# Kernel tuning notes

Measured on AMD Instinct MI355X. Metric: run time of the kernel, lower is better.

## Reference

```python
import jax, jax.numpy as jnp
import numpy as np

EPS = 1e-5
NUM_HEADS = 8
GN_GROUPS = 32


def _hardswish(x):
    return x * jnp.clip(x + 3.0, 0.0, 6.0) / 6.0


def setup_inputs() -> dict:
    key = jax.random.key(0)
    ks = jax.random.split(key, 12)
    B, C, H, W = 2, 256, 56, 56
    mid, inner = 32, 64  # mid_ca=max(C//8,32); inner=max(C//8, 8*8)//8*8
    s = 0.02
    return {
        "x": jax.random.normal(ks[0], (B, C, H, W), jnp.float32),
        "gate_conv_w": jax.random.normal(ks[1], (mid, C), jnp.float32) * s,
        "bn_gamma": jnp.ones((mid,), jnp.float32),
        "bn_beta": jnp.zeros((mid,), jnp.float32),
        "bn_mean": jax.random.normal(ks[2], (mid,), jnp.float32) * 0.1,
        "bn_var": jax.random.uniform(ks[3], (mid,), jnp.float32) + 0.5,
        "gate_h_w": jax.random.normal(ks[4], (C, mid), jnp.float32) * s,
        "gate_w_w": jax.random.normal(ks[5], (C, mid), jnp.float32) * s,
        "proj_in_w": jax.random.normal(ks[6], (inner, C), jnp.float32) * s,
        "ln_gamma": jnp.ones((inner,), jnp.float32),
        "ln_beta": jnp.zeros((inner,), jnp.float32),
        "wq": jax.random.normal(ks[7], (inner, inner), jnp.float32) * s,
        "wk": jax.random.normal(ks[8], (inner, inner), jnp.float32) * s,
        "wv": jax.random.normal(ks[9], (inner, inner), jnp.float32) * s,
        "proj_out_w": jax.random.normal(ks[10], (C, inner), jnp.float32) * s,
        "gn_gamma": jnp.ones((C,), jnp.float32),
        "gn_beta": jnp.zeros((C,), jnp.float32),
    }


def reference(x, gate_conv_w, bn_gamma, bn_beta, bn_mean, bn_var,
              gate_h_w, gate_w_w, proj_in_w, ln_gamma, ln_beta,
              wq, wk, wv, proj_out_w, gn_gamma, gn_beta):
    B, C, H, W = x.shape
    N = H * W
    inner = proj_in_w.shape[0]
    dh = inner // NUM_HEADS
    scale = dh ** (-0.5)

    # ---- CA gate: pool along W and H, shared 1x1 conv + BN(eval) + hardswish ----
    h_pool = x.mean(axis=3)                      # (B,C,H)
    w_pool = x.mean(axis=2)                      # (B,C,W)
    cat = jnp.concatenate([h_pool, w_pool], axis=2)          # (B,C,H+W)
    cat = jnp.einsum('mc,bcl->bml', gate_conv_w, cat)        # 1x1 conv
    cat = (cat - bn_mean[:, None]) * jax.lax.rsqrt(bn_var[:, None] + EPS)
    cat = cat * bn_gamma[:, None] + bn_beta[:, None]
    cat = _hardswish(cat)
    g_h, g_w = cat[:, :, :H], cat[:, :, H:]                  # (B,mid,H), (B,mid,W)
    gate_h = jax.nn.sigmoid(jnp.einsum('cm,bmh->bch', gate_h_w, g_h))  # (B,C,H)
    gate_w = jax.nn.sigmoid(jnp.einsum('cm,bmw->bcw', gate_w_w, g_w))  # (B,C,W)
    gate = gate_h[:, :, :, None] * gate_w[:, :, None, :]     # (B,C,H,W)

    # ---- projection + layernorm over channel dim ----
    seq = jnp.einsum('ic,bchw->bhwi', proj_in_w, x).reshape(B, N, inner)
    mu = seq.mean(-1, keepdims=True)
    var = seq.var(-1, keepdims=True)  # biased, as torch LayerNorm
    seq = (seq - mu) * jax.lax.rsqrt(var + EPS) * ln_gamma + ln_beta

    gate_spatial = gate.mean(axis=1).reshape(B, N)           # (B,N)

    def heads(w):
        return (seq @ w.T).reshape(B, N, NUM_HEADS, dh).transpose(0, 2, 1, 3)
    q, k, v = heads(wq), heads(wk), heads(wv)                # (B,h,N,dh)

    scores = jnp.einsum('bhnd,bhmd->bhnm', q, k) * scale     # (B,h,N,N)
    gate_bias = jnp.maximum(jnp.log(gate_spatial), -5.0)[:, None, None, :]
    attn = jax.nn.softmax(scores + gate_bias, axis=-1)
    out = jnp.einsum('bhnm,bhmd->bhnd', attn, v)             # (B,h,N,dh)
    out = out.transpose(0, 2, 1, 3).reshape(B, N, inner)
    out = out.transpose(0, 2, 1).reshape(B, inner, H, W)
    out = jnp.einsum('ci,bihw->bchw', proj_out_w, out)       # proj_out 1x1 conv

    # ---- GroupNorm(32, C) ----
    og = out.reshape(B, GN_GROUPS, C // GN_GROUPS, H, W)
    gmu = og.mean((2, 3, 4), keepdims=True)
    gvar = og.var((2, 3, 4), keepdims=True)
    og = (og - gmu) * jax.lax.rsqrt(gvar + EPS)
    out = og.reshape(B, C, H, W) * gn_gamma[None, :, None, None] + gn_beta[None, :, None, None]

    return x + out
```

## Files before the change

### kernel.cpp

```cpp
#include <hip/hip_runtime.h>
#include <math.h>

#define EPSF 1e-5f

constexpr int B_ = 2, C_ = 256, H_ = 56, W_ = 56, N_ = 3136;
constexpr int MID_ = 32, L_ = 112, IN_ = 64, NH_ = 8;

typedef __attribute__((ext_vector_type(8))) __bf16 bf16x8;
typedef __attribute__((ext_vector_type(16))) float f32x16;

constexpr size_t O_POOL = 0;
constexpr size_t O_CAT  = O_POOL + (size_t)B_*C_*L_;
constexpr size_t O_GH   = O_CAT  + (size_t)B_*MID_*L_;
constexpr size_t O_GW   = O_GH   + (size_t)B_*C_*H_;
constexpr size_t O_BIAS = O_GW   + (size_t)B_*C_*W_;
constexpr size_t O_QT   = O_BIAS + (size_t)B_*N_;
constexpr size_t O_KT   = O_QT   + (size_t)B_*NH_*N_*16/2;
constexpr size_t O_VT   = O_KT   + (size_t)B_*NH_*N_*16/2;
constexpr size_t O_VZ   = O_VT   + (size_t)B_*NH_*16*N_/2;
constexpr size_t O_AOT  = O_VZ   + N_/2;
constexpr size_t O_OUTC = O_AOT  + (size_t)B_*N_*IN_;
constexpr size_t O_GST  = O_OUTC + (size_t)B_*C_*N_;
constexpr size_t O_PART = O_GST  + (size_t)B_*32*2;

__device__ inline unsigned pkbf(float lo, float hi) {
  __bf16 a = (__bf16)lo, c = (__bf16)hi;
  return (unsigned)__builtin_bit_cast(unsigned short, a)
       | ((unsigned)__builtin_bit_cast(unsigned short, c) << 16);
}

__device__ inline float fast_exp2(float x) {
#if __has_builtin(__builtin_amdgcn_exp2f)
  return __builtin_amdgcn_exp2f(x);
#else
  float r; asm("v_exp_f32 %0, %1" : "=v"(r) : "v"(x)); return r;
#endif
}

__device__ inline void plane32_swap(unsigned &a, unsigned &b) {
#if __has_builtin(__builtin_amdgcn_permlane32_swap)
  typedef unsigned uv2 __attribute__((ext_vector_type(2)));
  uv2 r = __builtin_amdgcn_permlane32_swap(a, b, false, false);
  a = r.x; b = r.y;
#else
  asm volatile("v_permlane32_swap_b32 %0, %1" : "+v"(a), "+v"(b));
#endif
}

__global__ __launch_bounds__(256) void k_pool(const float* __restrict__ x, float* __restrict__ pool) {
  int bc = blockIdx.x;
  const float4* xp4 = reinterpret_cast<const float4*>(x + (size_t)bc * N_);
  __shared__ float tile[N_];
  float4* t4 = reinterpret_cast<float4*>(tile);
  for (int i = threadIdx.x; i < N_/4; i += 256) t4[i] = xp4[i];
  __syncthreads();
  int t = threadIdx.x;
  if (t < 224) {
    int o = t >> 1, half = t & 1;
    float r = 0.f;
    if (o < 56) {
      const float* row = tile + o*W_ + half*28;
      #pragma unroll 7
      for (int j = 0; j < 28; ++j) r += row[j];
    } else {
      const float* col = tile + (half*28)*W_ + (o - 56);
      #pragma unroll 7
      for (int j = 0; j < 28; ++j) r += col[j*W_];
    }
    r += __shfl_xor(r, 1);
    if (half == 0) pool[(size_t)bc*L_ + o] = r * (1.f/56.f);
  }
}

__global__ __launch_bounds__(256) void k_gates2(const float* __restrict__ gcw, const float* __restrict__ pool,
    const float* __restrict__ bng, const float* __restrict__ bnb,
    const float* __restrict__ bnm, const float* __restrict__ bnv,
    const float* __restrict__ ghw, const float* __restrict__ gww,
    float* __restrict__ ghT, float* __restrict__ gwT) {
  int b = blockIdx.x / H_;
  int p = blockIdx.x % H_;
  __shared__ float cat_s[2][MID_];
  int t = threadIdx.x;
  {
    int out = t >> 2, sub = t & 3;
    int m = out & 31, which = out >> 5;
    int l = p + which*H_;
    const float* pp = pool + (size_t)b*C_*L_ + l;
    const float* wp = gcw + (size_t)m*C_ + sub*64;
    float s = 0.f;
    #pragma unroll 16
    for (int c = 0; c < 64; ++c) s += wp[c] * pp[(size_t)(sub*64 + c)*L_];
    s += __shfl_xor(s, 1); s += __shfl_xor(s, 2);
    if (sub == 0) {
      float xn = (s - bnm[m]) * rsqrtf(bnv[m] + EPSF) * bng[m] + bnb[m];
      cat_s[which][m] = xn * fminf(fmaxf(xn + 3.f, 0.f), 6.f) * (1.f/6.f);
    }
  }
  __syncthreads();
  int c = t;
  float sh = 0.f, sw = 0.f;
  #pragma unroll 8
  for (int m = 0; m < MID_; ++m) {
    sh += ghw[c*MID_ + m] * cat_s[0][m];
    sw += gww[c*MID_ + m] * cat_s[1][m];
  }
  ghT[((size_t)b*H_ + p)*C_ + c] = 1.f/(1.f + expf(-sh));
  gwT[((size_t)b*W_ + p)*C_ + c] = 1.f/(1.f + expf(-sw));
}

__global__ __launch_bounds__(256) void k_bias(const float* __restrict__ ghT, const float* __restrict__ gwT,
                                              float* __restrict__ bias) {
  int wid = blockIdx.x*4 + (threadIdx.x >> 6);
  int lane = threadIdx.x & 63;
  int n = wid % N_, b = wid / N_;
  int h = n / W_, w = n % W_;
  float4 a  = *reinterpret_cast<const float4*>(ghT + ((size_t)b*H_ + h)*C_ + lane*4);
  float4 c2 = *reinterpret_cast<const float4*>(gwT + ((size_t)b*W_ + w)*C_ + lane*4);
  float s = a.x*c2.x + a.y*c2.y + a.z*c2.z + a.w*c2.w;
  s += __shfl_xor(s, 1);  s += __shfl_xor(s, 2);  s += __shfl_xor(s, 4);
  s += __shfl_xor(s, 8);  s += __shfl_xor(s, 16); s += __shfl_xor(s, 32);
  if (lane == 0)
    bias[(size_t)b*N_ + n] = fmaxf(logf(s * (1.f/C_)), -5.f) * 1.4426950408889634f;
}

__global__ __launch_bounds__(256) void k_fused(const float* __restrict__ x,
    const float* __restrict__ piw, const float* __restrict__ lng, const float* __restrict__ lnb,
    const float* __restrict__ wq, const float* __restrict__ wk, const float* __restrict__ wv,
    const float* __restrict__ bias,
    unsigned short* __restrict__ qt, unsigned short* __restrict__ kt,
    unsigned short* __restrict__ vt, unsigned short* __restrict__ vz) {
  __shared__ __align__(16) unsigned short sT[64][72];
  __shared__ float ps[2][2][64][2];
  __shared__ float lg[64], lb[64];
  int b = blockIdx.x / 49, n0 = (blockIdx.x % 49) * 64;
  int tid = threadIdx.x;
  int wv_ = tid >> 6, lane = tid & 63;
  int m = wv_ & 1, nh = wv_ >> 1, l31 = lane & 31, g = lane >> 5;
  int nloc = nh*32 + l31;
  int nglob = n0 + nloc;
  const float QS = 0.35355339059327373f * 1.4426950408889634f;

  if (tid < 64) { lg[tid] = lng[tid]; lb[tid] = lnb[tid]; }

  for (int u = tid; u < 512; u += 256) {
    int h = u >> 6, n = u & 63;
    size_t base = ((size_t)(b*NH_ + h)*N_ + n0 + n)*16;
    *reinterpret_cast<uint4*>(qt + base + 8) = make_uint4(0x3F803F80u, 0u, 0u, 0u);
    float bv = bias[(size_t)b*N_ + n0 + n];
    __bf16 bhi = (__bf16)bv; float blo = bv - (float)bhi;
    *reinterpret_cast<uint4*>(kt + base + 8) = make_uint4(pkbf((float)bhi, blo), 0u, 0u, 0u);
  }
  for (int u = tid; u < 512; u += 256) {
    int rr = u >> 3, chunk = u & 7;
    int h = rr >> 3, r = 8 + (rr & 7);
    unsigned val = (r == 8 || r == 12) ? 0x3F803F80u : 0u;
    *reinterpret_cast<uint4*>(vt + ((size_t)(b*NH_+h)*16 + r)*N_ + n0 + chunk*8)
        = make_uint4(val, val, val, val);
  }
  if (b == 0 && tid < 8)
    *reinterpret_cast<uint4*>(vz + n0 + tid*8) = make_uint4(0u, 0u, 0u, 0u);

  const float* arow = piw + (size_t)(32*m + l31)*C_;
  const float* xcol = x + (size_t)b*C_*N_ + nglob;
  f32x16 acc;
  #pragma unroll
  for (int i = 0; i < 16; ++i) acc[i] = 0.f;
  #pragma unroll 4
  for (int kk = 0; kk < 16; ++kk) {
    const float4* ap = reinterpret_cast<const float4*>(arow + kk*16 + g*8);
    float4 a0 = ap[0], a1 = ap[1];
    uint4 au;
    au.x = pkbf(a0.x, a0.y); au.y = pkbf(a0.z, a0.w);
    au.z = pkbf(a1.x, a1.y); au.w = pkbf(a1.z, a1.w);
    float bvl[8];
    #pragma unroll
    for (int e = 0; e < 8; ++e) bvl[e] = xcol[(size_t)(kk*16 + g*8 + e)*N_];
    uint4 bu;
    bu.x = pkbf(bvl[0], bvl[1]); bu.y = pkbf(bvl[2], bvl[3]);
    bu.z = pkbf(bvl[4], bvl[5]); bu.w = pkbf(bvl[6], bvl[7]);
    acc = __builtin_amdgcn_mfma_f32_32x32x16_bf16(
        __builtin_bit_cast(bf16x8, au), __builtin_bit_cast(bf16x8, bu), acc, 0, 0, 0);
  }

  float s = 0.f, ss = 0.f;
  #pragma unroll
  for (int i = 0; i < 16; ++i) { s += acc[i]; ss += acc[i]*acc[i]; }
  ps[m][g][nloc][0] = s; ps[m][g][nloc][1] = ss;
  __syncthreads();
  float S  = ps[0][0][nloc][0] + ps[0][1][nloc][0] + ps[1][0][nloc][0] + ps[1][1][nloc][0];
  float SS = ps[0][0][nloc][1] + ps[0][1][nloc][1] + ps[1][0][nloc][1] + ps[1][1][nloc][1];
  float mu = S * (1.f/IN_);
  float var = SS * (1.f/IN_) - mu*mu;
  float rsd = rsqrtf(var + EPSF);

  #pragma unroll
  for (int cg = 0; cg < 4; ++cg) {
    int jb = 8*cg + 4*g + 32*m;
    float v0 = (acc[cg*4+0]-mu)*rsd*lg[jb+0] + lb[jb+0];
    float v1 = (acc[cg*4+1]-mu)*rsd*lg[jb+1] + lb[jb+1];
    float v2 = (acc[cg*4+2]-mu)*rsd*lg[jb+2] + lb[jb+2];
    float v3 = (acc[cg*4+3]-mu)*rsd*lg[jb+3] + lb[jb+3];
    uint2 w; w.x = pkbf(v0, v1); w.y = pkbf(v2, v3);
    *reinterpret_cast<uint2*>(&sT[nloc][jb]) = w;
  }
  __syncthreads();

  f32x16 aq, ak, av;
  #pragma unroll
  for (int i = 0; i < 16; ++i) { aq[i] = 0.f; ak[i] = 0.f; av[i] = 0.f; }
  const float* qrw = wq + (size_t)(32*m + l31)*IN_;
  const float* krw = wk + (size_t)(32*m + l31)*IN_;
  const float* vrw = wv + (size_t)(32*m + l31)*IN_;
  #pragma unroll
  for (int kk = 0; kk < 4; ++kk) {
    bf16x8 bfr = __builtin_bit_cast(bf16x8,
        *reinterpret_cast<const uint4*>(&sT[nloc][kk*16 + g*8]));
    auto ldA = [&](const float* wrow) {
      const float4* fp = reinterpret_cast<const float4*>(wrow + kk*16 + g*8);
      float4 f0 = fp[0], f1 = fp[1];
      uint4 u;
      u.x = pkbf(f0.x, f0.y); u.y = pkbf(f0.z, f0.w);
      u.z = pkbf(f1.x, f1.y); u.w = pkbf(f1.z, f1.w);
      return __builtin_bit_cast(bf16x8, u);
    };
    aq = __builtin_amdgcn_mfma_f32_32x32x16_bf16(ldA(qrw), bfr, aq, 0, 0, 0);
    ak = __builtin_amdgcn_mfma_f32_32x32x16_bf16(ldA(krw), bfr, ak, 0, 0, 0);
    av = __builtin_amdgcn_mfma_f32_32x32x16_bf16(ldA(vrw), bfr, av, 0, 0, 0);
  }

  #pragma unroll
  for (int cg = 0; cg < 4; ++cg) {
    int h = 4*m + cg, d0 = 4*g;
    size_t rb = ((size_t)(b*NH_ + h)*N_ + nglob)*16 + d0;
    uint2 wqv;
    wqv.x = pkbf(aq[cg*4+0]*QS, aq[cg*4+1]*QS);
    wqv.y = pkbf(aq[cg*4+2]*QS, aq[cg*4+3]*QS);
    *reinterpret_cast<uint2*>(qt + rb) = wqv;
    uint2 wkv;
    wkv.x = pkbf(ak[cg*4+0], ak[cg*4+1]);
    wkv.y = pkbf(ak[cg*4+2], ak[cg*4+3]);
    *reinterpret_cast<uint2*>(kt + rb) = wkv;
    unsigned r0 = pkbf(av[cg*4+0], av[cg*4+1]);
    unsigned r1 = pkbf(av[cg*4+2], av[cg*4+3]);
    size_t vb0 = ((size_t)(b*NH_+h)*16 + d0)*N_ + nglob;
    vt[vb0]                = (unsigned short)r0;
    vt[vb0 + N_]           = (unsigned short)(r0 >> 16);
    vt[vb0 + 2*(size_t)N_] = (unsigned short)r1;
    vt[vb0 + 3*(size_t)N_] = (unsigned short)(r1 >> 16);
  }
}

__global__ __launch_bounds__(256, 4) void k_attn7(const unsigned short* __restrict__ qt,
    const unsigned short* __restrict__ kt, const unsigned short* __restrict__ vt,
    const unsigned short* __restrict__ vz, float* __restrict__ part_g) {
  int tid = threadIdx.x;
  int lane = tid & 63, kh = tid >> 6;
  int l31 = lane & 31, g = lane >> 5;
  int bh = blockIdx.x & 15;
  int rest = blockIdx.x >> 4;
  int qti = rest >> 1, half = rest & 1;
  int qbase = qti * 64;

  bf16x8 qfA = __builtin_bit_cast(bf16x8,
      *reinterpret_cast<const uint4*>(qt + ((size_t)bh*N_ + qbase + l31)*16 + g*8));
  bf16x8 qfB = __builtin_bit_cast(bf16x8,
      *reinterpret_cast<const uint4*>(qt + ((size_t)bh*N_ + qbase + 32 + l31)*16 + g*8));
  f32x16 zf, accA, accB;
  #pragma unroll
  for (int i = 0; i < 16; ++i) { zf[i] = 0.f; accA[i] = 0.f; accB[i] = 0.f; }
  const unsigned short* krow = kt + (size_t)bh*N_*16 + g*8;
  const unsigned short* vbase = (l31 < 16) ? (vt + ((size_t)bh*16 + l31)*(size_t)N_) : vz;

  auto ld = [&](const unsigned short* p) {
    return __builtin_bit_cast(bf16x8, *reinterpret_cast<const uint4*>(p));
  };
  auto halfstep = [&](const f32x16& sa, f32x16& acc, bf16x8 v1, bf16x8 v2) {
    float p[16];
    #pragma unroll
    for (int r = 0; r < 16; ++r) p[r] = fast_exp2(sa[r]);
    unsigned u01 = pkbf(p[0],p[1]),  u23 = pkbf(p[2],p[3]);
    unsigned u45 = pkbf(p[4],p[5]),  u67 = pkbf(p[6],p[7]);
    unsigned u89 = pkbf(p[8],p[9]),  uab = pkbf(p[10],p[11]);
    unsigned ucd = pkbf(p[12],p[13]), uef = pkbf(p[14],p[15]);
    plane32_swap(u01, u45);
    plane32_swap(u23, u67);
    plane32_swap(u89, ucd);
    plane32_swap(uab, uef);
    bf16x8 pf1 = __builtin_bit_cast(bf16x8, make_uint4(u01, u23, u45, u67));
    bf16x8 pf2 = __builtin_bit_cast(bf16x8, make_uint4(u89, uab, ucd, uef));
    acc = __builtin_amdgcn_mfma_f32_32x32x16_bf16(v1, pf1, acc, 0, 0, 0);
    acc = __builtin_amdgcn_mfma_f32_32x32x16_bf16(v2, pf2, acc, 0, 0, 0);
  };

  int tb0 = (half*49 + kh*12) * 32;
  const unsigned short* kp  = krow  + (size_t)(tb0 + l31)*16;
  const unsigned short* vp1 = vbase + tb0 + g*8;
  const unsigned short* vp2 = vp1 + 16;

  bf16x8 kfN = ld(kp), v1N = ld(vp1), v2N = ld(vp2);
  #pragma unroll 4
  for (int j = 0; j < 12; ++j) {
    bf16x8 kf = kfN, v1 = v1N, v2 = v2N;
    if (j < 11) {
      kfN = ld(kp  + (size_t)(j+1)*512);
      v1N = ld(vp1 + (j+1)*32);
      v2N = ld(vp2 + (j+1)*32);
    }
    f32x16 sA = __builtin_amdgcn_mfma_f32_32x32x16_bf16(kf, qfA, zf, 0, 0, 0);
    f32x16 sB = __builtin_amdgcn_mfma_f32_32x32x16_bf16(kf, qfB, zf, 0, 0, 0);
    halfstep(sA, accA, v1, v2);
    halfstep(sB, accB, v1, v2);
  }
  if (kh == 0) {
    int tb = (half*49 + 48) * 32;
    bf16x8 kf = ld(krow + (size_t)(tb + l31)*16);
    bf16x8 v1 = ld(vbase + tb + g*8);
    bf16x8 v2 = ld(vbase + tb + 16 + g*8);
    f32x16 sA = __builtin_amdgcn_mfma_f32_32x32x16_bf16(kf, qfA, zf, 0, 0, 0);
    f32x16 sB = __builtin_amdgcn_mfma_f32_32x32x16_bf16(kf, qfB, zf, 0, 0, 0);
    halfstep(sA, accA, v1, v2);
    halfstep(sB, accB, v1, v2);
  }

  __shared__ float part[3][2][64][5];
  if (kh > 0) {
    #pragma unroll
    for (int j = 0; j < 5; ++j) {
      part[kh-1][0][lane][j] = accA[j];
      part[kh-1][1][lane][j] = accB[j];
    }
  }
  __syncthreads();
  if (kh == 0) {
    float rA[5], rB[5];
    #pragma unroll
    for (int j = 0; j < 5; ++j) { rA[j] = accA[j]; rB[j] = accB[j]; }
    #pragma unroll
    for (int c = 0; c < 3; ++c) {
      #pragma unroll
      for (int j = 0; j < 5; ++j) {
        rA[j] += part[c][0][lane][j];
        rB[j] += part[c][1][lane][j];
      }
    }
    float* pg = part_g + ((((size_t)half*16 + bh)*2 + g)*5)*N_ + qbase + l31;
    #pragma unroll
    for (int j = 0; j < 5; ++j) {
      pg[(size_t)j*N_]      = rA[j];
      pg[(size_t)j*N_ + 32] = rB[j];
    }
  }
}

__global__ __launch_bounds__(128) void k_proj3(const float* __restrict__ part_g,
    const float* __restrict__ pw, float* __restrict__ outc, float* __restrict__ gst) {
  int bid = blockIdx.x;
  int nb = bid % 49, ct = (bid / 49) % 8, b = bid / (49*8);
  int wave = threadIdx.x >> 6, lane = threadIdx.x & 63;
  int l31 = lane & 31, g = lane >> 5;
  int n0 = nb*64, c0 = ct*32;
  int nw = n0 + wave*32;

  __shared__ float invs[8][64];
  for (int u = threadIdx.x; u < 512; u += 128) {
    int h = u >> 6, n = u & 63;
    size_t r0 = ((((size_t)0*16 + b*8 + h)*2 + 0)*5 + 4)*N_ + n0 + n;
    size_t r1 = ((((size_t)1*16 + b*8 + h)*2 + 0)*5 + 4)*N_ + n0 + n;
    invs[h][n] = 1.f / (part_g[r0] + part_g[r1]);
  }
  __syncthreads();

  const float* wrow = pw + (size_t)(c0 + l31)*IN_;
  bf16x8 afr[4];
  #pragma unroll
  for (int kk = 0; kk < 4; ++kk) {
    const float4* fp = reinterpret_cast<const float4*>(wrow + kk*16 + g*8);
    float4 f0 = fp[0], f1 = fp[1];
    uint4 u;
    u.x = pkbf(f0.x, f0.y); u.y = pkbf(f0.z, f0.w);
    u.z = pkbf(f1.x, f1.y); u.w = pkbf(f1.z, f1.w);
    afr[kk] = __builtin_bit_cast(bf16x8, u);
  }

  f32x16 acc;
  #pragma unroll
  for (int i = 0; i < 16; ++i) acc[i] = 0.f;
  #pragma unroll
  for (int kk = 0; kk < 4; ++kk) {
    int h = kk*2 + g;
    float iv = invs[h][wave*32 + l31];
    const float* p0 = part_g + (((size_t)0*16 + b*8 + h)*2)*5*N_ + nw + l31;
    const float* p1 = part_g + (((size_t)1*16 + b*8 + h)*2)*5*N_ + nw + l31;
    unsigned words[4];
    #pragma unroll
    for (int ep = 0; ep < 4; ++ep) {
      float vv[2];
      #pragma unroll
      for (int e2 = 0; e2 < 2; ++e2) {
        int d = ep*2 + e2;
        int gr = d >> 2, j = d & 3;
        size_t off = ((size_t)gr*5 + j)*N_;
        vv[e2] = (p0[off] + p1[off]) * iv;
      }
      words[ep] = pkbf(vv[0], vv[1]);
    }
    uint4 bu = make_uint4(words[0], words[1], words[2], words[3]);
    acc = __builtin_amdgcn_mfma_f32_32x32x16_bf16(afr[kk], __builtin_bit_cast(bf16x8, bu), acc, 0, 0, 0);
  }

  float* op = outc + ((size_t)b*C_ + c0)*N_ + nw + l31;
  #pragma unroll
  for (int reg = 0; reg < 16; ++reg) {
    int row = (reg & 3) + 8*(reg >> 2) + 4*g;
    op[(size_t)row*N_] = acc[reg];
  }

  float s4[4], q4[4];
  #pragma unroll
  for (int gl = 0; gl < 4; ++gl) {
    s4[gl] = acc[gl*4+0] + acc[gl*4+1] + acc[gl*4+2] + acc[gl*4+3];
    q4[gl] = acc[gl*4+0]*acc[gl*4+0] + acc[gl*4+1]*acc[gl*4+1]
           + acc[gl*4+2]*acc[gl*4+2] + acc[gl*4+3]*acc[gl*4+3];
  }
  #pragma unroll
  for (int gl = 0; gl < 4; ++gl) {
    #pragma unroll
    for (int off = 32; off > 0; off >>= 1) {
      s4[gl] += __shfl_xor(s4[gl], off);
      q4[gl] += __shfl_xor(q4[gl], off);
    }
  }
  __shared__ float red[2][4][2];
  if (lane == 0) {
    #pragma unroll
    for (int gl = 0; gl < 4; ++gl) { red[wave][gl][0] = s4[gl]; red[wave][gl][1] = q4[gl]; }
  }
  __syncthreads();
  if (threadIdx.x < 8) {
    int gl = threadIdx.x >> 1, which = threadIdx.x & 1;
    float v = red[0][gl][which] + red[1][gl][which];
    atomicAdd(&gst[((size_t)b*32 + ct*4 + gl)*2 + which], v);
  }
}

__global__ __launch_bounds__(256) void k_final(const float* __restrict__ x, const float* __restrict__ outc,
    const float* __restrict__ gst, const float* __restrict__ gng, const float* __restrict__ gnb,
    float* __restrict__ out) {
  int tid = blockIdx.x*256 + threadIdx.x;
  size_t idx = (size_t)tid * 4;
  int c = (int)((idx / N_) % C_);
  int b = (int)(idx / ((size_t)C_*N_));
  int g = c >> 3;
  float S  = gst[(b*32+g)*2];
  float SS = gst[(b*32+g)*2+1];
  const float invn = 1.f/(8.f*N_);
  float mu = S * invn;
  float var = SS * invn - mu*mu;
  float rs = rsqrtf(var + EPSF);
  float ga = gng[c], be = gnb[c];
  float4 xv = *reinterpret_cast<const float4*>(x + idx);
  float4 ov = *reinterpret_cast<const float4*>(outc + idx);
  float4 r;
  r.x = xv.x + (ov.x - mu)*rs*ga + be;
  r.y = xv.y + (ov.y - mu)*rs*ga + be;
  r.z = xv.z + (ov.z - mu)*rs*ga + be;
  r.w = xv.w + (ov.w - mu)*rs*ga + be;
  *reinterpret_cast<float4*>(out + idx) = r;
}

extern "C" void kernel_launch(void* const* d_in, const int* in_sizes, int n_in,
                              void* d_out, int out_size, void* d_ws, size_t ws_size,
                              hipStream_t stream) {
  const float* x   = (const float*)d_in[0];
  const float* gcw = (const float*)d_in[1];
  const float* bng = (const float*)d_in[2];
  const float* bnb = (const float*)d_in[3];
  const float* bnm = (const float*)d_in[4];
  const float* bnv = (const float*)d_in[5];
  const float* ghw = (const float*)d_in[6];
  const float* gww = (const float*)d_in[7];
  const float* piw = (const float*)d_in[8];
  const float* lng = (const float*)d_in[9];
  const float* lnb = (const float*)d_in[10];
  const float* wq  = (const float*)d_in[11];
  const float* wk  = (const float*)d_in[12];
  const float* wv  = (const float*)d_in[13];
  const float* pw  = (const float*)d_in[14];
  const float* gng = (const float*)d_in[15];
  const float* gnb = (const float*)d_in[16];
  float* ws  = (float*)d_ws;
  float* out = (float*)d_out;
  unsigned short* qt  = (unsigned short*)(ws + O_QT);
  unsigned short* kt  = (unsigned short*)(ws + O_KT);
  unsigned short* vt  = (unsigned short*)(ws + O_VT);
  unsigned short* vz  = (unsigned short*)(ws + O_VZ);

  hipMemsetAsync(ws + O_GST, 0, (size_t)B_*32*2*sizeof(float), stream);
  k_pool<<<B_*C_, 256, 0, stream>>>(x, ws + O_POOL);
  k_gates2<<<B_*H_, 256, 0, stream>>>(gcw, ws+O_POOL, bng, bnb, bnm, bnv, ghw, gww, ws+O_GH, ws+O_GW);
  k_bias<<<(B_*N_)/4, 256, 0, stream>>>(ws+O_GH, ws+O_GW, ws+O_BIAS);
  k_fused<<<B_*49, 256, 0, stream>>>(x, piw, lng, lnb, wq, wk, wv, ws+O_BIAS, qt, kt, vt, vz);
  k_attn7<<<16*98, 256, 0, stream>>>(qt, kt, vt, vz, ws+O_PART);
  k_proj3<<<B_*8*49, 128, 0, stream>>>(ws+O_PART, pw, ws+O_OUTC, ws+O_GST);
  k_final<<<(B_*C_*N_)/(4*256), 256, 0, stream>>>(x, ws+O_OUTC, ws+O_GST, gng, gnb, out);
}
```

Baseline: 84.14 us.

## Fuse gate bias into k_fused, drop memset, store proj_out in bf16

Folds the spatial gate-bias computation into k_fused: each block computes its 64 pixels' bias from ghT/gwT into shared memory. This removes the k_bias launch and its global round trip. The GroupNorm stats buffer is now zeroed inside k_fused instead of by a separate memset. The proj_out intermediate is stored as bf16 instead of fp32, halving its write and read traffic in k_proj3 and k_final. The risk is some precision loss in the residual output, while the GroupNorm stats stay computed from fp32 accumulators.

```diff
diff --git a/kernel.cpp b/kernel.cpp
--- a/kernel.cpp
+++ b/kernel.cpp
@@ -10,23 +10,25 @@
 typedef __attribute__((ext_vector_type(16))) float f32x16;
 
 constexpr size_t O_POOL = 0;
-constexpr size_t O_CAT  = O_POOL + (size_t)B_*C_*L_;
-constexpr size_t O_GH   = O_CAT  + (size_t)B_*MID_*L_;
+constexpr size_t O_GH   = O_POOL + (size_t)B_*C_*L_;
 constexpr size_t O_GW   = O_GH   + (size_t)B_*C_*H_;
-constexpr size_t O_BIAS = O_GW   + (size_t)B_*C_*W_;
-constexpr size_t O_QT   = O_BIAS + (size_t)B_*N_;
+constexpr size_t O_QT   = O_GW   + (size_t)B_*C_*W_;
 constexpr size_t O_KT   = O_QT   + (size_t)B_*NH_*N_*16/2;
 constexpr size_t O_VT   = O_KT   + (size_t)B_*NH_*N_*16/2;
 constexpr size_t O_VZ   = O_VT   + (size_t)B_*NH_*16*N_/2;
-constexpr size_t O_AOT  = O_VZ   + N_/2;
-constexpr size_t O_OUTC = O_AOT  + (size_t)B_*N_*IN_;
-constexpr size_t O_GST  = O_OUTC + (size_t)B_*C_*N_;
+constexpr size_t O_OUTC = O_VZ   + N_/2;
+constexpr size_t O_GST  = O_OUTC + (size_t)B_*C_*N_/2;
 constexpr size_t O_PART = O_GST  + (size_t)B_*32*2;
 
 __device__ inline unsigned pkbf(float lo, float hi) {
   __bf16 a = (__bf16)lo, c = (__bf16)hi;
   return (unsigned)__builtin_bit_cast(unsigned short, a)
        | ((unsigned)__builtin_bit_cast(unsigned short, c) << 16);
+}
+
+__device__ inline float bf2f(unsigned short u) {
+  unsigned v = (unsigned)u << 16;
+  return __builtin_bit_cast(float, v);
 }
 
 __device__ inline float fast_exp2(float x) {
@@ -108,30 +110,17 @@
   gwT[((size_t)b*W_ + p)*C_ + c] = 1.f/(1.f + expf(-sw));
 }
 
-__global__ __launch_bounds__(256) void k_bias(const float* __restrict__ ghT, const float* __restrict__ gwT,
-                                              float* __restrict__ bias) {
-  int wid = blockIdx.x*4 + (threadIdx.x >> 6);
-  int lane = threadIdx.x & 63;
-  int n = wid % N_, b = wid / N_;
-  int h = n / W_, w = n % W_;
-  float4 a  = *reinterpret_cast<const float4*>(ghT + ((size_t)b*H_ + h)*C_ + lane*4);
-  float4 c2 = *reinterpret_cast<const float4*>(gwT + ((size_t)b*W_ + w)*C_ + lane*4);
-  float s = a.x*c2.x + a.y*c2.y + a.z*c2.z + a.w*c2.w;
-  s += __shfl_xor(s, 1);  s += __shfl_xor(s, 2);  s += __shfl_xor(s, 4);
-  s += __shfl_xor(s, 8);  s += __shfl_xor(s, 16); s += __shfl_xor(s, 32);
-  if (lane == 0)
-    bias[(size_t)b*N_ + n] = fmaxf(logf(s * (1.f/C_)), -5.f) * 1.4426950408889634f;
-}
-
 __global__ __launch_bounds__(256) void k_fused(const float* __restrict__ x,
     const float* __restrict__ piw, const float* __restrict__ lng, const float* __restrict__ lnb,
     const float* __restrict__ wq, const float* __restrict__ wk, const float* __restrict__ wv,
-    const float* __restrict__ bias,
+    const float* __restrict__ ghT, const float* __restrict__ gwT,
     unsigned short* __restrict__ qt, unsigned short* __restrict__ kt,
-    unsigned short* __restrict__ vt, unsigned short* __restrict__ vz) {
+    unsigned short* __restrict__ vt, unsigned short* __restrict__ vz,
+    float* __restrict__ gst) {
   __shared__ __align__(16) unsigned short sT[64][72];
   __shared__ float ps[2][2][64][2];
   __shared__ float lg[64], lb[64];
+  __shared__ float bias_s[64];
   int b = blockIdx.x / 49, n0 = (blockIdx.x % 49) * 64;
   int tid = threadIdx.x;
   int wv_ = tid >> 6, lane = tid & 63;
@@ -141,12 +130,31 @@
   const float QS = 0.35355339059327373f * 1.4426950408889634f;
 
   if (tid < 64) { lg[tid] = lng[tid]; lb[tid] = lnb[tid]; }
+  if (blockIdx.x == 0 && tid < B_*32*2) gst[tid] = 0.f;
+
+  {
+    int px = tid >> 2, sub = tid & 3;
+    int n = n0 + px;
+    int h = n / W_, w = n % W_;
+    const float4* gh4 = reinterpret_cast<const float4*>(ghT + ((size_t)b*H_ + h)*C_ + sub*64);
+    const float4* gw4 = reinterpret_cast<const float4*>(gwT + ((size_t)b*W_ + w)*C_ + sub*64);
+    float s = 0.f;
+    #pragma unroll
+    for (int i = 0; i < 16; ++i) {
+      float4 a = gh4[i], c2 = gw4[i];
+      s += a.x*c2.x + a.y*c2.y + a.z*c2.z + a.w*c2.w;
+    }
+    s += __shfl_xor(s, 1); s += __shfl_xor(s, 2);
+    if (sub == 0)
+      bias_s[px] = fmaxf(logf(s * (1.f/C_)), -5.f) * 1.4426950408889634f;
+  }
+  __syncthreads();
 
   for (int u = tid; u < 512; u += 256) {
     int h = u >> 6, n = u & 63;
     size_t base = ((size_t)(b*NH_ + h)*N_ + n0 + n)*16;
     *reinterpret_cast<uint4*>(qt + base + 8) = make_uint4(0x3F803F80u, 0u, 0u, 0u);
-    float bv = bias[(size_t)b*N_ + n0 + n];
+    float bv = bias_s[n];
     __bf16 bhi = (__bf16)bv; float blo = bv - (float)bhi;
     *reinterpret_cast<uint4*>(kt + base + 8) = make_uint4(pkbf((float)bhi, blo), 0u, 0u, 0u);
   }
@@ -353,7 +361,7 @@
 }
 
 __global__ __launch_bounds__(128) void k_proj3(const float* __restrict__ part_g,
-    const float* __restrict__ pw, float* __restrict__ outc, float* __restrict__ gst) {
+    const float* __restrict__ pw, unsigned short* __restrict__ outc, float* __restrict__ gst) {
   int bid = blockIdx.x;
   int nb = bid % 49, ct = (bid / 49) % 8, b = bid / (49*8);
   int wave = threadIdx.x >> 6, lane = threadIdx.x & 63;
@@ -408,11 +416,12 @@
     acc = __builtin_amdgcn_mfma_f32_32x32x16_bf16(afr[kk], __builtin_bit_cast(bf16x8, bu), acc, 0, 0, 0);
   }
 
-  float* op = outc + ((size_t)b*C_ + c0)*N_ + nw + l31;
+  unsigned short* op = outc + ((size_t)b*C_ + c0)*N_ + nw + l31;
   #pragma unroll
   for (int reg = 0; reg < 16; ++reg) {
     int row = (reg & 3) + 8*(reg >> 2) + 4*g;
-    op[(size_t)row*N_] = acc[reg];
+    __bf16 vb = (__bf16)acc[reg];
+    op[(size_t)row*N_] = __builtin_bit_cast(unsigned short, vb);
   }
 
   float s4[4], q4[4];
@@ -443,9 +452,9 @@
   }
 }
 
-__global__ __launch_bounds__(256) void k_final(const float* __restrict__ x, const float* __restrict__ outc,
-    const float* __restrict__ gst, const float* __restrict__ gng, const float* __restrict__ gnb,
-    float* __restrict__ out) {
+__global__ __launch_bounds__(256) void k_final(const float* __restrict__ x,
+    const unsigned short* __restrict__ outc, const float* __restrict__ gst,
+    const float* __restrict__ gng, const float* __restrict__ gnb, float* __restrict__ out) {
   int tid = blockIdx.x*256 + threadIdx.x;
   size_t idx = (size_t)tid * 4;
   int c = (int)((idx / N_) % C_);
@@ -459,12 +468,16 @@
   float rs = rsqrtf(var + EPSF);
   float ga = gng[c], be = gnb[c];
   float4 xv = *reinterpret_cast<const float4*>(x + idx);
-  float4 ov = *reinterpret_cast<const float4*>(outc + idx);
+  uint2 ou = *reinterpret_cast<const uint2*>(outc + idx);
+  float o0 = bf2f((unsigned short)(ou.x & 0xffff));
+  float o1 = bf2f((unsigned short)(ou.x >> 16));
+  float o2 = bf2f((unsigned short)(ou.y & 0xffff));
+  float o3 = bf2f((unsigned short)(ou.y >> 16));
   float4 r;
-  r.x = xv.x + (ov.x - mu)*rs*ga + be;
-  r.y = xv.y + (ov.y - mu)*rs*ga + be;
-  r.z = xv.z + (ov.z - mu)*rs*ga + be;
-  r.w = xv.w + (ov.w - mu)*rs*ga + be;
+  r.x = xv.x + (o0 - mu)*rs*ga + be;
+  r.y = xv.y + (o1 - mu)*rs*ga + be;
+  r.z = xv.z + (o2 - mu)*rs*ga + be;
+  r.w = xv.w + (o3 - mu)*rs*ga + be;
   *reinterpret_cast<float4*>(out + idx) = r;
 }
 
@@ -490,17 +503,17 @@
   const float* gnb = (const float*)d_in[16];
   float* ws  = (float*)d_ws;
   float* out = (float*)d_out;
-  unsigned short* qt  = (unsigned short*)(ws + O_QT);
-  unsigned short* kt  = (unsigned short*)(ws + O_KT);
-  unsigned short* vt  = (unsigned short*)(ws + O_VT);
-  unsigned short* vz  = (unsigned short*)(ws + O_VZ);
-
-  hipMemsetAsync(ws + O_GST, 0, (size_t)B_*32*2*sizeof(float), stream);
+  unsigned short* qt   = (unsigned short*)(ws + O_QT);
+  unsigned short* kt   = (unsigned short*)(ws + O_KT);
+  unsigned short* vt   = (unsigned short*)(ws + O_VT);
+  unsigned short* vz   = (unsigned short*)(ws + O_VZ);
+  unsigned short* outc = (unsigned short*)(ws + O_OUTC);
+
   k_pool<<<B_*C_, 256, 0, stream>>>(x, ws + O_POOL);
   k_gates2<<<B_*H_, 256, 0, stream>>>(gcw, ws+O_POOL, bng, bnb, bnm, bnv, ghw, gww, ws+O_GH, ws+O_GW);
-  k_bias<<<(B_*N_)/4, 256, 0, stream>>>(ws+O_GH, ws+O_GW, ws+O_BIAS);
-  k_fused<<<B_*49, 256, 0, stream>>>(x, piw, lng, lnb, wq, wk, wv, ws+O_BIAS, qt, kt, vt, vz);
+  k_fused<<<B_*49, 256, 0, stream>>>(x, piw, lng, lnb, wq, wk, wv, ws+O_GH, ws+O_GW,
+                                     qt, kt, vt, vz, ws+O_GST);
   k_attn7<<<16*98, 256, 0, stream>>>(qt, kt, vt, vz, ws+O_PART);
-  k_proj3<<<B_*8*49, 128, 0, stream>>>(ws+O_PART, pw, ws+O_OUTC, ws+O_GST);
-  k_final<<<(B_*C_*N_)/(4*256), 256, 0, stream>>>(x, ws+O_OUTC, ws+O_GST, gng, gnb, out);
-}
+  k_proj3<<<B_*8*49, 128, 0, stream>>>(ws+O_PART, pw, outc, ws+O_GST);
+  k_final<<<(B_*C_*N_)/(4*256), 256, 0, stream>>>(x, outc, ws+O_GST, gng, gnb, out);
+}
```

Result: faster. 80.57 us (-4.2%).
